# Kernel optimization log

Measured on AMD Instinct MI355X. Metric: run time of the kernel, lower is better.

## Reference

```python
import jax, jax.numpy as jnp
import numpy as np

B, N, IN_DIM, OUT_DIM, H = 8, 1024, 256, 256, 8
D = OUT_DIM // H  # head_dim = 32
NEG_INF = -1.0e9


def setup_inputs() -> dict:
    key = jax.random.key(0)
    k_x, k_adj, k_W, k_a = jax.random.split(key, 4)
    x = jax.random.normal(k_x, (B, N, IN_DIM), dtype=jnp.float32)
    adj = jax.random.randint(k_adj, (B, N, N), 0, 2, dtype=jnp.int32)
    # nn.Linear(in_dim, out_dim, bias=False): weight [out_dim, in_dim]
    lim = 1.0 / np.sqrt(IN_DIM)
    W = jax.random.uniform(k_W, (OUT_DIM, IN_DIM), jnp.float32, -lim, lim)
    # a: (1, H, 2*D), xavier_uniform with gain=1.414
    gain = 1.414
    bound = gain * np.sqrt(6.0 / (H + 2 * D))
    a = jax.random.uniform(k_a, (1, H, 2 * D), jnp.float32, -bound, bound)
    return {"x": x, "adj": adj, "W": W, "a": a}


def reference(x, adj, W, a):
    Bn, Nn, _ = x.shape
    h = jnp.einsum('bni,oi->bno', x, W).reshape(Bn, Nn, H, D)  # [B,N,H,D]
    # sum(cat(h_i, h_j) * a) = h_i . a_src + h_j . a_dst  (avoids O(N^2*2D) concat)
    a_src = a[0, :, :D]   # [H,D] multiplies h_i (query/row index i)
    a_dst = a[0, :, D:]   # [H,D] multiplies h_j (key/col index j)
    s_i = jnp.einsum('bnhd,hd->bnh', h, a_src)  # [B,N,H]
    s_j = jnp.einsum('bnhd,hd->bnh', h, a_dst)  # [B,N,H]
    e = s_i[:, :, None, :] + s_j[:, None, :, :]  # [B,i,j,H]
    e = jnp.where(e > 0, e, 0.2 * e)  # LeakyReLU(0.2)
    mask = (adj != 0)[..., None]      # [B,N,N,1] broadcast over heads
    e = jnp.where(mask, e, NEG_INF)
    alpha = jax.nn.softmax(e, axis=2)  # softmax over j (neighbors)
    # dropout p=0.0 -> identity
    h_prime = jnp.einsum('bijh,bjhd->bihd', alpha, h)
    h_prime = h_prime.reshape(Bn, Nn, H * D)
    return jax.nn.elu(h_prime)
```

## Files before the change

kernel.cpp:

```cpp
#include <hip/hip_runtime.h>
#include <cmath>

namespace {
constexpr int B = 8, N = 1024, IND = 256, OUTD = 256, H = 8, D = 32;
constexpr float LOG2E = 1.4426950408889634f;
}

typedef __attribute__((ext_vector_type(8))) short short8v;
typedef __attribute__((ext_vector_type(4))) float f32x4;

__device__ inline ushort f2bf(float f) {
  __bf16 b = (__bf16)f;
  return __builtin_bit_cast(ushort, b);
}
__device__ inline float bf2f(ushort u) {
  return __uint_as_float((uint)u << 16);
}

__global__ __launch_bounds__(256) void gat_k1(
    const float* __restrict__ x, const float* __restrict__ W,
    const float* __restrict__ a, const int* __restrict__ adj,
    uint* __restrict__ bitsT, float* __restrict__ siT,
    float* __restrict__ sjT, ushort* __restrict__ hTbF) {
  const int bid = blockIdx.x;
  const int t = threadIdx.x;

  if (bid >= 512) {
    const int lane = t & 63, w = t >> 6;
    const int wid = (bid - 512) * 4 + w;
    const int b = wid >> 10, i = wid & 1023;
    const int4* ap = (const int4*)(adj + ((size_t)b * N + i) * N);
#pragma unroll
    for (int c = 0; c < 4; ++c) {
      const int4 v = ap[c * 64 + lane];
      uint val = (v.x != 0 ? 1u : 0u) | (v.y != 0 ? 2u : 0u) |
                 (v.z != 0 ? 4u : 0u) | (v.w != 0 ? 8u : 0u);
      val <<= (lane & 7) * 4;
      val |= (uint)__shfl_xor((int)val, 1);
      val |= (uint)__shfl_xor((int)val, 2);
      val |= (uint)__shfl_xor((int)val, 4);
      if ((lane & 7) == 0) {
        const int jt = c * 8 + (lane >> 3);
        bitsT[((size_t)b * 32 + jt) * N + i] = val;
      }
    }
    return;
  }

  __shared__ __align__(16) char smem[17664];
  float(*xs)[36] = (float(*)[36])smem;
  ushort* wsh = (ushort*)(smem + 9216);
  ushort* wsl = (ushort*)(smem + 13312);
  float(*tile2)[65] = (float(*)[65])smem;

  const int lane = t & 63, w = t >> 6;
  const int la = lane & 15, g = lane >> 4;
  const int work = ((bid & 7) << 6) + (bid >> 3);
  const int bx = work >> 2, by = work & 3;

  f32x4 z = {0.f, 0.f, 0.f, 0.f};
  f32x4 acc[4] = {z, z, z, z};

  const float* xp = x + (size_t)(bx * 64 + (t >> 2)) * IND + (t & 3) * 8;
  const int w_c = by * 64 + (t >> 6) * 16 + (t & 15);
  const int w_k0 = ((t >> 4) & 3) * 8;
  const float* wp = W + (size_t)w_c * IND + w_k0;

  for (int kb = 0; kb < 8; ++kb) {
    __syncthreads();
    {
      float4 v0 = *(const float4*)(xp + kb * 32);
      float4 v1 = *(const float4*)(xp + kb * 32 + 4);
      float* dst = &xs[t >> 2][(t & 3) * 8];
      *(float4*)dst = v0;
      *(float4*)(dst + 4) = v1;
    }
    {
      float4 v0 = *(const float4*)(wp + kb * 32);
      float4 v1 = *(const float4*)(wp + kb * 32 + 4);
      const float wf[8] = {v0.x, v0.y, v0.z, v0.w, v1.x, v1.y, v1.z, v1.w};
      short8v ph, pl;
#pragma unroll
      for (int e = 0; e < 8; ++e) {
        const ushort hi = f2bf(wf[e]);
        ph[e] = (short)hi;
        pl[e] = (short)f2bf(wf[e] - bf2f(hi));
      }
      *(short8v*)&wsh[t * 8] = ph;
      *(short8v*)&wsl[t * 8] = pl;
    }
    __syncthreads();

    const float* xr = &xs[w * 16 + la][g * 8];
    float4 u0 = *(const float4*)(xr);
    float4 u1 = *(const float4*)(xr + 4);
    const float af[8] = {u0.x, u0.y, u0.z, u0.w, u1.x, u1.y, u1.z, u1.w};
    short8v ah, al;
#pragma unroll
    for (int e = 0; e < 8; ++e) {
      const ushort hb = f2bf(af[e]);
      ah[e] = (short)hb;
      al[e] = (short)f2bf(af[e] - bf2f(hb));
    }
#pragma unroll
    for (int ct = 0; ct < 4; ++ct) {
      const short8v bh = *(const short8v*)&wsh[ct * 512 + lane * 8];
      const short8v bl = *(const short8v*)&wsl[ct * 512 + lane * 8];
      acc[ct] = __builtin_amdgcn_mfma_f32_16x16x32_bf16(ah, bh, acc[ct], 0, 0, 0);
      acc[ct] = __builtin_amdgcn_mfma_f32_16x16x32_bf16(al, bh, acc[ct], 0, 0, 0);
      acc[ct] = __builtin_amdgcn_mfma_f32_16x16x32_bf16(ah, bl, acc[ct], 0, 0, 0);
    }
  }

  const int batch = bx >> 4;
  const int nbase = (bx & 15) * 64 + w * 16;

#pragma unroll
  for (int hp2 = 0; hp2 < 2; ++hp2) {
    const int head = by * 2 + hp2;
    const float a0 = a[head * 64 + la] * LOG2E;
    const float a1 = a[head * 64 + 16 + la] * LOG2E;
    const float a2 = a[head * 64 + 32 + la] * LOG2E;
    const float a3 = a[head * 64 + 48 + la] * LOG2E;
    float s1v[4], s2v[4];
#pragma unroll
    for (int q = 0; q < 4; ++q) {
      s1v[q] = acc[hp2 * 2][q] * a0 + acc[hp2 * 2 + 1][q] * a1;
      s2v[q] = acc[hp2 * 2][q] * a2 + acc[hp2 * 2 + 1][q] * a3;
    }
#pragma unroll
    for (int mask = 1; mask <= 8; mask <<= 1)
#pragma unroll
      for (int q = 0; q < 4; ++q) {
        s1v[q] += __shfl_xor(s1v[q], mask);
        s2v[q] += __shfl_xor(s2v[q], mask);
      }
    if (la == 0) {
#pragma unroll
      for (int q = 0; q < 4; ++q) {
        const size_t o = (size_t)(batch * H + head) * N + nbase + g * 4 + q;
        siT[o] = s1v[q];
        sjT[o] = s2v[q];
      }
    }
  }

  __syncthreads();
#pragma unroll
  for (int ct = 0; ct < 4; ++ct)
#pragma unroll
    for (int q = 0; q < 4; ++q)
      tile2[w * 16 + g * 4 + q][ct * 16 + la] = acc[ct][q];
  __syncthreads();

  const int jt0 = (bx & 15) * 2;
#pragma unroll
  for (int s = 0; s < 2; ++s) {
    const int gg = t * 2 + s;
    const int head = gg >> 8, rem = gg & 255;
    const int jt_loc = rem >> 7, half = (rem >> 6) & 1, l = rem & 63;
    const int d = half * 16 + (l & 15);
    short8v pk;
#pragma unroll
    for (int e = 0; e < 8; ++e)
      pk[e] = (short)f2bf(tile2[jt_loc * 32 + (l >> 4) * 8 + e][head * 32 + d]);
    const int bh_g = batch * H + by * 2 + head;
    *(short8v*)(hTbF + ((size_t)(bh_g * 32 + jt0 + jt_loc) * 64 + l) * 16 + half * 8) = pk;
  }
}

__global__ __launch_bounds__(256) void gat_agg(
    const uint* __restrict__ bitsT, const float* __restrict__ siT,
    const float* __restrict__ sjT, const ushort* __restrict__ hTbF,
    float* __restrict__ out) {
  __shared__ float sj_lds[1024];
  __shared__ uint bits_lds[32][32];
  __shared__ float part[2][64][13];
  const int t = threadIdx.x;
  const int lane = t & 63, w = t >> 6;
  const int iw = w & 1, jq = w >> 1;
  const int bid = blockIdx.x;
  const int work = ((bid & 7) << 8) + (bid >> 3);
  const int bh = work >> 5;
  const int itg = work & 31;
  const int b = bh >> 3, hh = bh & 7;
  const int i0 = itg * 32 + iw * 16;
  const int la = lane & 15, g = lane >> 4;
  const int iA = i0 + la;

  const float si_r = siT[(size_t)bh * N + iA];

  {
    float4 v = *(const float4*)(sjT + (size_t)bh * N + t * 4);
    *(float4*)&sj_lds[t * 4] = v;
    const int jt = t >> 3, c4 = (t & 7) * 4;
    uint4 bv = *(const uint4*)(bitsT + ((size_t)b * 32 + jt) * N + itg * 32 + c4);
    *(uint4*)&bits_lds[jt][c4] = bv;
  }
  __syncthreads();

  const ushort* hp = hTbF + (size_t)bh * 32768 + (size_t)jq * 16384 + lane * 16;
  const uint* blp = &bits_lds[jq * 16][iw * 16 + la];
  const float* slp = &sj_lds[jq * 512 + g * 8];

  f32x4 acc0 = {0.f, 0.f, 0.f, 0.f}, acc1 = {0.f, 0.f, 0.f, 0.f};
  f32x4 accl = {0.f, 0.f, 0.f, 0.f};
  short8v ones;
#pragma unroll
  for (int e = 0; e < 8; ++e) ones[e] = (short)0x3F80;

  uint bits_A, bits_B;
  float4 sj0A, sj1A, sj0B, sj1B;
  short8v h0A, h1A, h0B, h1B;

#define AGG_LDS(S, JT)                                     \
  bits_##S = blp[(JT)*32];                                 \
  sj0##S = *(const float4*)(slp + (JT) * 32);              \
  sj1##S = *(const float4*)(slp + (JT) * 32 + 4);

#define AGG_LOAD_H(S, JT)                                  \
  h0##S = *(const short8v*)(hp + (size_t)(JT)*1024);       \
  h1##S = *(const short8v*)(hp + (size_t)(JT)*1024 + 8);

#define AGG_COMP(S)                                                           \
  {                                                                           \
    const uint byte_ = (bits_##S >> (g * 8)) & 0xffu;                         \
    const float sjv[8] = {sj0##S.x, sj0##S.y, sj0##S.z, sj0##S.w,             \
                          sj1##S.x, sj1##S.y, sj1##S.z, sj1##S.w};            \
    short8v af;                                                               \
    _Pragma("unroll") for (int e = 0; e < 8; ++e) {                           \
      float s = si_r + sjv[e];                                                \
      s = fmaxf(s, 0.2f * s);                                                 \
      s = ((byte_ >> e) & 1u) ? s : -INFINITY;                                \
      af[e] = (short)f2bf(__builtin_amdgcn_exp2f(s));                         \
    }                                                                         \
    __builtin_amdgcn_s_setprio(1);                                            \
    acc0 = __builtin_amdgcn_mfma_f32_16x16x32_bf16(af, h0##S, acc0, 0, 0, 0); \
    acc1 = __builtin_amdgcn_mfma_f32_16x16x32_bf16(af, h1##S, acc1, 0, 0, 0); \
    accl = __builtin_amdgcn_mfma_f32_16x16x32_bf16(af, ones, accl, 0, 0, 0);  \
    __builtin_amdgcn_s_setprio(0);                                            \
  }

  AGG_LDS(A, 0)
  AGG_LOAD_H(A, 0)
  AGG_LDS(B, 1)
  AGG_LOAD_H(B, 1)
#pragma unroll
  for (int jt = 0; jt < 16; jt += 2) {
    AGG_COMP(A)
    if (jt + 2 < 16) { AGG_LDS(A, jt + 2) AGG_LOAD_H(A, jt + 2) }
    AGG_COMP(B)
    if (jt + 3 < 16) { AGG_LDS(B, jt + 3) AGG_LOAD_H(B, jt + 3) }
  }
#undef AGG_LDS
#undef AGG_LOAD_H
#undef AGG_COMP

  if (jq == 1) {
    float* p = part[iw][lane];
#pragma unroll
    for (int k = 0; k < 4; ++k) {
      p[k] = acc0[k];
      p[4 + k] = acc1[k];
      p[8 + k] = accl[k];
    }
  }
  __syncthreads();
  if (jq == 0) {
    const float* p = part[iw][lane];
#pragma unroll
    for (int k = 0; k < 4; ++k) {
      acc0[k] += p[k];
      acc1[k] += p[4 + k];
      accl[k] += p[8 + k];
    }
    float* op = out + ((size_t)(b * N + i0)) * OUTD + hh * D;
#pragma unroll
    for (int r = 0; r < 4; ++r) {
      const int ic = g * 4 + r;
      const float li = accl[r];
      float v0 = acc0[r] / li;
      v0 = v0 > 0.f ? v0 : expm1f(v0);
      op[(size_t)ic * OUTD + la] = v0;
      float v1 = acc1[r] / li;
      v1 = v1 > 0.f ? v1 : expm1f(v1);
      op[(size_t)ic * OUTD + 16 + la] = v1;
    }
  }
}

extern "C" void kernel_launch(void* const* d_in, const int* in_sizes, int n_in,
                              void* d_out, int out_size, void* d_ws, size_t ws_size,
                              hipStream_t stream) {
  const float* x = (const float*)d_in[0];
  const int* adj = (const int*)d_in[1];
  const float* W = (const float*)d_in[2];
  const float* a = (const float*)d_in[3];
  float* out = (float*)d_out;

  float* ws = (float*)d_ws;
  float* siT = ws;
  float* sjT = siT + (size_t)B * N * H;
  uint* bitsT = (uint*)(sjT + (size_t)B * N * H);
  ushort* hTbF = (ushort*)(bitsT + (size_t)B * 32 * N);

  gat_k1<<<512 + 2048, 256, 0, stream>>>(x, W, a, adj, bitsT, siT, sjT, hTbF);
  gat_agg<<<2048, 256, 0, stream>>>(bitsT, siT, sjT, hTbF, out);
}
```

Baseline: 41.60 us.

## Software-pipeline attention weight build against MFMAs in GAT aggregation loop

Restructures the aggregation inner loop so that the exp/mask construction of the next tile's attention fragment is interleaved with the MFMAs of the current tile. Loads are clamped to the last tile index instead of being guarded by conditionals, and the setprio hints are dropped. Adds a launch_bounds occupancy hint of 6 waves per EU. The aim is to overlap VALU work with matrix-core work and to raise occupancy, at the cost of extra live registers and a few redundant loads at the tail.

Result: slower. 42.47 us (+2.1%).

```diff
diff --git a/kernel.cpp b/kernel.cpp
--- a/kernel.cpp
+++ b/kernel.cpp
@@ -169,7 +169,7 @@
   }
 }
 
-__global__ __launch_bounds__(256) void gat_agg(
+__global__ __launch_bounds__(256, 6) void gat_agg(
     const uint* __restrict__ bitsT, const float* __restrict__ siT,
     const float* __restrict__ sjT, const ushort* __restrict__ hTbF,
     float* __restrict__ out) {
@@ -209,52 +209,71 @@
 #pragma unroll
   for (int e = 0; e < 8; ++e) ones[e] = (short)0x3F80;
 
-  uint bits_A, bits_B;
-  float4 sj0A, sj1A, sj0B, sj1B;
-  short8v h0A, h1A, h0B, h1B;
-
-#define AGG_LDS(S, JT)                                     \
-  bits_##S = blp[(JT)*32];                                 \
-  sj0##S = *(const float4*)(slp + (JT) * 32);              \
-  sj1##S = *(const float4*)(slp + (JT) * 32 + 4);
-
-#define AGG_LOAD_H(S, JT)                                  \
-  h0##S = *(const short8v*)(hp + (size_t)(JT)*1024);       \
-  h1##S = *(const short8v*)(hp + (size_t)(JT)*1024 + 8);
-
-#define AGG_COMP(S)                                                           \
+  uint bits_P, bits_Q;
+  float4 sj0P, sj1P, sj0Q, sj1Q;
+  short8v h0P, h1P, h0Q, h1Q;
+  short8v af_c, af_n;
+
+#define CL15(X) ((X) > 15 ? 15 : (X))
+
+#define LDS_P(JT)                                   \
+  bits_P = blp[CL15(JT) * 32];                      \
+  sj0P = *(const float4*)(slp + CL15(JT) * 32);     \
+  sj1P = *(const float4*)(slp + CL15(JT) * 32 + 4);
+#define LDS_Q(JT)                                   \
+  bits_Q = blp[CL15(JT) * 32];                      \
+  sj0Q = *(const float4*)(slp + CL15(JT) * 32);     \
+  sj1Q = *(const float4*)(slp + CL15(JT) * 32 + 4);
+#define LDH_P(JT)                                            \
+  h0P = *(const short8v*)(hp + (size_t)CL15(JT) * 1024);     \
+  h1P = *(const short8v*)(hp + (size_t)CL15(JT) * 1024 + 8);
+#define LDH_Q(JT)                                            \
+  h0Q = *(const short8v*)(hp + (size_t)CL15(JT) * 1024);     \
+  h1Q = *(const short8v*)(hp + (size_t)CL15(JT) * 1024 + 8);
+
+#define BUILD(AF, BITS, SJ0, SJ1)                                             \
   {                                                                           \
-    const uint byte_ = (bits_##S >> (g * 8)) & 0xffu;                         \
-    const float sjv[8] = {sj0##S.x, sj0##S.y, sj0##S.z, sj0##S.w,             \
-                          sj1##S.x, sj1##S.y, sj1##S.z, sj1##S.w};            \
-    short8v af;                                                               \
+    const uint byte_ = ((BITS) >> (g * 8)) & 0xffu;                           \
+    const float sjv[8] = {(SJ0).x, (SJ0).y, (SJ0).z, (SJ0).w,                 \
+                          (SJ1).x, (SJ1).y, (SJ1).z, (SJ1).w};                \
     _Pragma("unroll") for (int e = 0; e < 8; ++e) {                           \
       float s = si_r + sjv[e];                                                \
       s = fmaxf(s, 0.2f * s);                                                 \
       s = ((byte_ >> e) & 1u) ? s : -INFINITY;                                \
-      af[e] = (short)f2bf(__builtin_amdgcn_exp2f(s));                         \
+      AF[e] = (short)f2bf(__builtin_amdgcn_exp2f(s));                         \
     }                                                                         \
-    __builtin_amdgcn_s_setprio(1);                                            \
-    acc0 = __builtin_amdgcn_mfma_f32_16x16x32_bf16(af, h0##S, acc0, 0, 0, 0); \
-    acc1 = __builtin_amdgcn_mfma_f32_16x16x32_bf16(af, h1##S, acc1, 0, 0, 0); \
-    accl = __builtin_amdgcn_mfma_f32_16x16x32_bf16(af, ones, accl, 0, 0, 0);  \
-    __builtin_amdgcn_s_setprio(0);                                            \
-  }
-
-  AGG_LDS(A, 0)
-  AGG_LOAD_H(A, 0)
-  AGG_LDS(B, 1)
-  AGG_LOAD_H(B, 1)
+  }
+
+#define MFMA3(AF, H0, H1)                                                     \
+  acc0 = __builtin_amdgcn_mfma_f32_16x16x32_bf16(AF, H0, acc0, 0, 0, 0);      \
+  acc1 = __builtin_amdgcn_mfma_f32_16x16x32_bf16(AF, H1, acc1, 0, 0, 0);      \
+  accl = __builtin_amdgcn_mfma_f32_16x16x32_bf16(AF, ones, accl, 0, 0, 0);
+
+  LDS_Q(0)
+  LDS_P(1)
+  LDH_P(0)
+  LDH_Q(1)
+  BUILD(af_c, bits_Q, sj0Q, sj1Q)
+  LDS_Q(2)
+
 #pragma unroll
   for (int jt = 0; jt < 16; jt += 2) {
-    AGG_COMP(A)
-    if (jt + 2 < 16) { AGG_LDS(A, jt + 2) AGG_LOAD_H(A, jt + 2) }
-    AGG_COMP(B)
-    if (jt + 3 < 16) { AGG_LDS(B, jt + 3) AGG_LOAD_H(B, jt + 3) }
-  }
-#undef AGG_LDS
-#undef AGG_LOAD_H
-#undef AGG_COMP
+    BUILD(af_n, bits_P, sj0P, sj1P)
+    MFMA3(af_c, h0P, h1P)
+    LDS_P(jt + 3)
+    LDH_P(jt + 2)
+    BUILD(af_c, bits_Q, sj0Q, sj1Q)
+    MFMA3(af_n, h0Q, h1Q)
+    LDS_Q(jt + 4)
+    LDH_Q(jt + 3)
+  }
+#undef CL15
+#undef LDS_P
+#undef LDS_Q
+#undef LDH_P
+#undef LDH_Q
+#undef BUILD
+#undef MFMA3
 
   if (jq == 1) {
     float* p = part[iw][lane];
```
